# Optimization experiments

Hardware: AMD Instinct MI355X
Metric: run time of the kernel (lower is better)

The kernel has to match this reference:

```python
import jax, jax.numpy as jnp
import numpy as np

EPS = 1e-11
NUM_ITERATIONS = 3


def squash(t, axis=-1):
    # squared norm along axis, squash scale = |s|^2/(1+|s|^2)
    sq = jnp.sum(t * t, axis=axis, keepdims=True)
    scale = sq / (1.0 + sq)
    unit = t / jnp.sqrt(sq + EPS)
    return scale * unit, scale


def setup_inputs() -> dict:
    key = jax.random.key(0)
    kx, ka, kw, kal = jax.random.split(key, 4)
    B, Nl, Nh, Din, Dout, K = 32, 256, 16, 16, 32, 8
    x = jax.random.normal(kx, (B, Nl, Din, Din), dtype=jnp.float32)
    adj = jax.random.normal(ka, (B, Nl, Nl), dtype=jnp.float32)  # unused by forward
    W = jax.random.normal(kw, (K, Din, Dout), dtype=jnp.float32)
    alpha = jax.random.normal(kal, (Nl, Nh, K), dtype=jnp.float32)
    return {"x": x, "adj": adj, "W": W, "alpha": alpha}


def reference(x, adj, W, alpha):
    B, Nl, Din, _ = x.shape
    Nh = alpha.shape[1]
    Dout = W.shape[2]
    # tmp2 = sum_k W[k] * alpha[l,h,k]  -> (Nl, Nh, Din, Dout)
    tmp2 = jnp.einsum('kio,lhk->lhio', W, alpha)
    # u_hat: per lower-capsule matrix times transform -> (B, Nl, Nh, Din, Dout)
    u = jnp.einsum('blri,lhio->blhro', x, tmp2)
    D = Din * Dout
    u_hat = u.reshape(B, Nl, Nh, D)  # capsule vector dim flattened (trailing 1 dropped)

    # dynamic routing on detached u_hat
    uh = jax.lax.stop_gradient(u_hat)
    b = jnp.zeros((B, Nl, Nh, 1), dtype=u_hat.dtype)
    for _ in range(NUM_ITERATIONS - 1):
        c = jax.nn.softmax(b, axis=2)               # over higher capsules
        s = jnp.sum(c * uh, axis=1, keepdims=True)  # (B,1,Nh,D)
        v, _ = squash(s, axis=-1)
        b = b + jnp.sum(uh * v, axis=-1, keepdims=True)  # agreement u_hat^T v
    c = jax.nn.softmax(b, axis=2)

    # final weighted sum with non-detached u_hat
    s = jnp.sum(c * u_hat, axis=1, keepdims=True)   # (B,1,Nh,D)
    v, a = squash(s, axis=-1)
    # match original shapes: v (B,1,Nh,D,1), a_j (B,1,Nh,1,1)
    return v[..., None], a[..., None]
```

## Files before the change

### kernel.cpp

```cpp
#include <hip/hip_runtime.h>
#include <hip/hip_bf16.h>

#define B_     32
#define NL     256
#define NH     16
#define DD     512
#define KK     8
#define LPB    32
#define NLC    (NL / LPB)
#define CHUNK  4
#define PSTR   24

typedef _Float16 f16;
typedef __attribute__((ext_vector_type(8)))  f16   f16x8;
typedef __attribute__((ext_vector_type(16))) float f32x16;

#define LO_SCALE 1024.0f
#define LO_INV   (1.0f / 1024.0f)

__device__ __forceinline__ void split2s(float f, f16& h, f16& l) {
    h = (f16)f;
    l = (f16)((f - (float)h) * LO_SCALE);
}

__global__ __launch_bounds__(512)
void tmp2_kernel(const float* __restrict__ W, const float* __restrict__ alpha,
                 f16* __restrict__ t2h, f16* __restrict__ t2l) {
    const int lh = blockIdx.x, d = threadIdx.x;
    const float* a = alpha + lh * KK;
    float acc = 0.f;
#pragma unroll
    for (int k = 0; k < KK; ++k) acc = fmaf(a[k], W[k * DD + d], acc);
    f16 h, l; split2s(acc, h, l);
    const size_t tt = (size_t)lh * DD + (d & 31) * 16 + (d >> 5);
    t2h[tt] = h; t2l[tt] = l;
}

template <int MODE>
__global__ __launch_bounds__(64)
void reduce_kernel(const float* __restrict__ spart, float* __restrict__ vbuf,
                   float* __restrict__ out_v, float* __restrict__ out_a) {
    const int bh = blockIdx.x, t = threadIdx.x;
    const float cs = (MODE == 0) ? (1.0f / 16.0f) : 1.0f;
    float acc[8];
#pragma unroll
    for (int j = 0; j < 8; ++j) acc[j] = 0.f;
    for (int ls = 0; ls < NLC; ++ls) {
        const float* p = spart + ((size_t)ls * (B_ * NH) + bh) * DD + t * 8;
        const float4 u0 = *(const float4*)&p[0];
        const float4 u1 = *(const float4*)&p[4];
        acc[0] += u0.x; acc[1] += u0.y; acc[2] += u0.z; acc[3] += u0.w;
        acc[4] += u1.x; acc[5] += u1.y; acc[6] += u1.z; acc[7] += u1.w;
    }
#pragma unroll
    for (int j = 0; j < 8; ++j) acc[j] *= cs;
    float sq = 0.f;
#pragma unroll
    for (int j = 0; j < 8; ++j) sq = fmaf(acc[j], acc[j], sq);
#pragma unroll
    for (int mm = 1; mm < 64; mm <<= 1) sq += __shfl_xor(sq, mm, 64);
    const float scale = sq / (1.0f + sq);
    const float inv   = scale / sqrtf(sq + 1e-11f);
    float* po = (MODE == 2) ? (out_v + (size_t)bh * DD + t * 8)
                            : (vbuf + (size_t)bh * DD + t * 8);
#pragma unroll
    for (int j = 0; j < 8; ++j) po[j] = acc[j] * inv;
    if (MODE == 2 && t == 0) out_a[bh] = scale;
}

template <int MODE>
__global__ __launch_bounds__(1024)
void pass_kernel(const float* __restrict__ x,
                 const f16* __restrict__ t2h, const f16* __restrict__ t2l,
                 const float* __restrict__ vbuf, float* __restrict__ blog,
                 float* __restrict__ spart) {
    __shared__ __align__(16) f16 xsh[LPB * 16 * PSTR];
    __shared__ __align__(16) f16 xsl[LPB * 16 * PSTR];
    __shared__ float dotsL[2][CHUNK][16];

    const int t  = threadIdx.x;
    const int b  = blockIdx.x >> 3, lc = blockIdx.x & 7;
    const int l0 = lc * LPB;
    const int wv = t >> 6, lane = t & 63;
    const int o  = lane & 31, l5 = lane >> 5;
    const int i0 = l5 * 8;
    const int rA = lane & 15;

    {
        const int row = t >> 1, half = t & 1;
        const float* xg = x + ((size_t)b * NL + l0 + (row >> 4)) * 256
                            + (row & 15) * 16 + half * 8;
        float xv[8];
        *(float4*)&xv[0] = *(const float4*)&xg[0];
        *(float4*)&xv[4] = *(const float4*)&xg[4];
        f16 hi[8], lo[8];
#pragma unroll
        for (int j = 0; j < 8; ++j) split2s(xv[j], hi[j], lo[j]);
        const int la = row * PSTR + half * 8;
        *(f16x8*)&xsh[la] = *(f16x8*)&hi[0];
        *(f16x8*)&xsl[la] = *(f16x8*)&lo[0];
    }
    __syncthreads();

    float vr[8];
    if (MODE != 0) {
        const float* vp = vbuf + ((size_t)b * NH + wv) * DD;
#pragma unroll
        for (int j = 0; j < 8; ++j) {
            const int rr = (j & 3) + 8 * (j >> 2) + 4 * l5;
            vr[j] = vp[rr * 32 + o];
        }
    }

    f16x8 pf0, pf1;
    {
        const size_t tb = ((size_t)l0 * NH + wv) * DD + o * 16 + i0;
        pf0 = *(const f16x8*)(t2h + tb);
        pf1 = *(const f16x8*)(t2l + tb);
    }

    float sacc[8];
#pragma unroll
    for (int j = 0; j < 8; ++j) sacc[j] = 0.f;

    for (int ch = 0; ch < LPB / CHUNK; ++ch) {
        const int par = ch & 1;
        float blg = 0.f;
        if (MODE == 2)
            blg = blog[((size_t)b * NL + l0 + ch * CHUNK + (lane >> 4)) * NH + (lane & 15)];

        float Pst[CHUNK][8];
#pragma unroll
        for (int lq = 0; lq < CHUNK; ++lq) {
            const int l = ch * CHUNK + lq;
            const int la = (l * 16 + rA) * PSTR + i0;
            const f16x8 a0 = *(const f16x8*)&xsh[la];
            const f16x8 a1 = *(const f16x8*)&xsl[la];
            const f16x8 c0 = pf0, c1 = pf1;
            if (l + 1 < LPB) {
                const size_t tb = ((size_t)(l0 + l + 1) * NH + wv) * DD + o * 16 + i0;
                pf0 = *(const f16x8*)(t2h + tb);
                pf1 = *(const f16x8*)(t2l + tb);
            }
            f32x16 z;
#pragma unroll
            for (int j = 0; j < 16; ++j) z[j] = 0.f;
            f32x16 c00 = __builtin_amdgcn_mfma_f32_32x32x16_f16(a0, c0, z, 0, 0, 0);
            f32x16 c01 = __builtin_amdgcn_mfma_f32_32x32x16_f16(a0, c1, z, 0, 0, 0);
            f32x16 c10 = __builtin_amdgcn_mfma_f32_32x32x16_f16(a1, c0, z, 0, 0, 0);
            float d0 = 0.f;
#pragma unroll
            for (int j = 0; j < 8; ++j) {
                const float pj = fmaf(c01[j] + c10[j], LO_INV, c00[j]);
                if (MODE != 0) { Pst[lq][j] = pj; d0 = fmaf(pj, vr[j], d0); }
                else           sacc[j] += pj;
            }
            if (MODE != 0) {
#pragma unroll
                for (int mm = 1; mm < 64; mm <<= 1) d0 += __shfl_xor(d0, mm, 64);
                if (lane == 0) dotsL[par][lq][wv] = d0;
            }
        }

        if (MODE != 0) {
            __syncthreads();
            float d = dotsL[par][lane >> 4][lane & 15];
            if (MODE == 2) d += blg;
            if (MODE == 1 && wv == 0)
                blog[((size_t)b * NL + l0 + ch * CHUNK + (lane >> 4)) * NH + (lane & 15)] = d;
            float mx = d;
#pragma unroll
            for (int mm = 1; mm < 16; mm <<= 1) mx = fmaxf(mx, __shfl_xor(mx, mm, 16));
            const float e = __expf(d - mx);
            float sm = e;
#pragma unroll
            for (int mm = 1; mm < 16; mm <<= 1) sm += __shfl_xor(sm, mm, 16);
            const float cv = e / sm;
#pragma unroll
            for (int lq = 0; lq < CHUNK; ++lq) {
                const float c = __shfl(cv, lq * 16 + wv, 64);
#pragma unroll
                for (int j = 0; j < 8; ++j)
                    sacc[j] = fmaf(c, Pst[lq][j], sacc[j]);
            }
        }
    }

    {
        float* sp = spart + ((size_t)lc * (B_ * NH) + b * NH + wv) * DD;
#pragma unroll
        for (int j = 0; j < 8; ++j) {
            const int rr = (j & 3) + 8 * (j >> 2) + 4 * l5;
            sp[rr * 32 + o] = sacc[j];
        }
    }
}

extern "C" void kernel_launch(void* const* d_in, const int* in_sizes, int n_in,
                              void* d_out, int out_size, void* d_ws, size_t ws_size,
                              hipStream_t stream) {
    const float* x     = (const float*)d_in[0];
    const float* W     = (const float*)d_in[2];
    const float* alpha = (const float*)d_in[3];
    float* out   = (float*)d_out;
    float* out_v = out;
    float* out_a = out + (size_t)B_ * NH * DD;

    char* base = (char*)d_ws;
    size_t off = 0;
    f16*   t2h   = (f16*)(base + off);   off += (size_t)NL * NH * DD * 2;
    f16*   t2l   = (f16*)(base + off);   off += (size_t)NL * NH * DD * 2;
    float* spart = (float*)(base + off); off += (size_t)NLC * B_ * NH * DD * 4;
    float* vbuf  = (float*)(base + off); off += (size_t)B_ * NH * DD * 4;
    float* blogp = (float*)(base + off); off += (size_t)B_ * NL * NH * 4;

    tmp2_kernel<<<NL * NH, 512, 0, stream>>>(W, alpha, t2h, t2l);

    const int grid = B_ * NLC;
    pass_kernel<0><<<grid, 1024, 0, stream>>>(x, t2h, t2l, vbuf, blogp, spart);
    reduce_kernel<0><<<B_ * NH, 64, 0, stream>>>(spart, vbuf, nullptr, nullptr);

    pass_kernel<1><<<grid, 1024, 0, stream>>>(x, t2h, t2l, vbuf, blogp, spart);
    reduce_kernel<1><<<B_ * NH, 64, 0, stream>>>(spart, vbuf, nullptr, nullptr);

    pass_kernel<2><<<grid, 1024, 0, stream>>>(x, t2h, t2l, vbuf, blogp, spart);
    reduce_kernel<2><<<B_ * NH, 64, 0, stream>>>(spart, nullptr, out_v, out_a);
}
```

Before: 162.2 us.

## Fuse all routing passes into one persistent kernel with grid barriers

Replaces the seven separate launches (tmp2, three pass kernels, three reduce kernels) with a single persistent kernel of 256 blocks. Global atomic-counter barriers separate the tmp2 build, each routing pass and each squash reduction. Routing logits now stay in shared memory instead of a global buffer. The aim is to remove launch gaps and global round-trips, at the cost of relying on all 256 blocks being co-resident and paying for spin-wait barriers.

```diff
diff --git a/kernel.cpp b/kernel.cpp
--- a/kernel.cpp
+++ b/kernel.cpp
@@ -7,9 +7,10 @@
 #define DD     512
 #define KK     8
 #define LPB    32
-#define NLC    (NL / LPB)
+#define NLC    8
 #define CHUNK  4
 #define PSTR   24
+#define NBLK   256
 
 typedef _Float16 f16;
 typedef __attribute__((ext_vector_type(8)))  f16   f16x8;
@@ -23,68 +24,58 @@
     l = (f16)((f - (float)h) * LO_SCALE);
 }
 
-__global__ __launch_bounds__(512)
-void tmp2_kernel(const float* __restrict__ W, const float* __restrict__ alpha,
-                 f16* __restrict__ t2h, f16* __restrict__ t2l) {
-    const int lh = blockIdx.x, d = threadIdx.x;
-    const float* a = alpha + lh * KK;
-    float acc = 0.f;
-#pragma unroll
-    for (int k = 0; k < KK; ++k) acc = fmaf(a[k], W[k * DD + d], acc);
-    f16 h, l; split2s(acc, h, l);
-    const size_t tt = (size_t)lh * DD + (d & 31) * 16 + (d >> 5);
-    t2h[tt] = h; t2l[tt] = l;
-}
-
-template <int MODE>
-__global__ __launch_bounds__(64)
-void reduce_kernel(const float* __restrict__ spart, float* __restrict__ vbuf,
-                   float* __restrict__ out_v, float* __restrict__ out_a) {
-    const int bh = blockIdx.x, t = threadIdx.x;
-    const float cs = (MODE == 0) ? (1.0f / 16.0f) : 1.0f;
-    float acc[8];
-#pragma unroll
-    for (int j = 0; j < 8; ++j) acc[j] = 0.f;
-    for (int ls = 0; ls < NLC; ++ls) {
-        const float* p = spart + ((size_t)ls * (B_ * NH) + bh) * DD + t * 8;
-        const float4 u0 = *(const float4*)&p[0];
-        const float4 u1 = *(const float4*)&p[4];
-        acc[0] += u0.x; acc[1] += u0.y; acc[2] += u0.z; acc[3] += u0.w;
-        acc[4] += u1.x; acc[5] += u1.y; acc[6] += u1.z; acc[7] += u1.w;
-    }
-#pragma unroll
-    for (int j = 0; j < 8; ++j) acc[j] *= cs;
-    float sq = 0.f;
-#pragma unroll
-    for (int j = 0; j < 8; ++j) sq = fmaf(acc[j], acc[j], sq);
-#pragma unroll
-    for (int mm = 1; mm < 64; mm <<= 1) sq += __shfl_xor(sq, mm, 64);
-    const float scale = sq / (1.0f + sq);
-    const float inv   = scale / sqrtf(sq + 1e-11f);
-    float* po = (MODE == 2) ? (out_v + (size_t)bh * DD + t * 8)
-                            : (vbuf + (size_t)bh * DD + t * 8);
-#pragma unroll
-    for (int j = 0; j < 8; ++j) po[j] = acc[j] * inv;
-    if (MODE == 2 && t == 0) out_a[bh] = scale;
-}
-
-template <int MODE>
-__global__ __launch_bounds__(1024)
-void pass_kernel(const float* __restrict__ x,
-                 const f16* __restrict__ t2h, const f16* __restrict__ t2l,
-                 const float* __restrict__ vbuf, float* __restrict__ blog,
-                 float* __restrict__ spart) {
+__device__ __forceinline__ void gbar(unsigned* cnt, int id) {
+    __syncthreads();
+    if (threadIdx.x == 0) {
+        __threadfence();
+        atomicAdd(&cnt[id], 1u);
+        while (__hip_atomic_load(&cnt[id], __ATOMIC_RELAXED,
+                                 __HIP_MEMORY_SCOPE_AGENT) < NBLK)
+            __builtin_amdgcn_s_sleep(2);
+        __threadfence();
+    }
+    __syncthreads();
+}
+
+__global__ __launch_bounds__(1024, 4)
+void fused_kernel(const float* __restrict__ x, const float* __restrict__ W,
+                  const float* __restrict__ alpha,
+                  f16* __restrict__ t2h, f16* __restrict__ t2l,
+                  float* __restrict__ vbuf, float* __restrict__ spart,
+                  unsigned* __restrict__ cnt,
+                  float* __restrict__ out_v, float* __restrict__ out_a) {
     __shared__ __align__(16) f16 xsh[LPB * 16 * PSTR];
     __shared__ __align__(16) f16 xsl[LPB * 16 * PSTR];
     __shared__ float dotsL[2][CHUNK][16];
+    __shared__ float blogS[LPB][16];
 
     const int t  = threadIdx.x;
-    const int b  = blockIdx.x >> 3, lc = blockIdx.x & 7;
+    const int lc = blockIdx.x >> 5, b = blockIdx.x & 31;
     const int l0 = lc * LPB;
     const int wv = t >> 6, lane = t & 63;
     const int o  = lane & 31, l5 = lane >> 5;
     const int i0 = l5 * 8;
     const int rA = lane & 15;
+
+    {
+        const int l = lc * 32 + b;
+        const int d = t & 511;
+        float wr[KK];
+#pragma unroll
+        for (int k = 0; k < KK; ++k) wr[k] = W[k * DD + d];
+        const size_t tbase = (size_t)l * NH * DD + ((d & 31) * 16 + (d >> 5));
+#pragma unroll
+        for (int e = 0; e < 8; ++e) {
+            const int h = 2 * e + (t >> 9);
+            const float* al = alpha + ((size_t)l * NH + h) * KK;
+            float acc = 0.f;
+#pragma unroll
+            for (int k = 0; k < KK; ++k) acc = fmaf(al[k], wr[k], acc);
+            f16 hh, ll; split2s(acc, hh, ll);
+            t2h[tbase + (size_t)h * DD] = hh;
+            t2l[tbase + (size_t)h * DD] = ll;
+        }
+    }
 
     {
         const int row = t >> 1, half = t & 1;
@@ -100,99 +91,129 @@
         *(f16x8*)&xsh[la] = *(f16x8*)&hi[0];
         *(f16x8*)&xsl[la] = *(f16x8*)&lo[0];
     }
-    __syncthreads();
-
-    float vr[8];
-    if (MODE != 0) {
-        const float* vp = vbuf + ((size_t)b * NH + wv) * DD;
-#pragma unroll
-        for (int j = 0; j < 8; ++j) {
-            const int rr = (j & 3) + 8 * (j >> 2) + 4 * l5;
-            vr[j] = vp[rr * 32 + o];
-        }
-    }
-
-    f16x8 pf0, pf1;
-    {
-        const size_t tb = ((size_t)l0 * NH + wv) * DD + o * 16 + i0;
-        pf0 = *(const f16x8*)(t2h + tb);
-        pf1 = *(const f16x8*)(t2l + tb);
-    }
-
-    float sacc[8];
-#pragma unroll
-    for (int j = 0; j < 8; ++j) sacc[j] = 0.f;
-
-    for (int ch = 0; ch < LPB / CHUNK; ++ch) {
-        const int par = ch & 1;
-        float blg = 0.f;
-        if (MODE == 2)
-            blg = blog[((size_t)b * NL + l0 + ch * CHUNK + (lane >> 4)) * NH + (lane & 15)];
-
-        float Pst[CHUNK][8];
-#pragma unroll
-        for (int lq = 0; lq < CHUNK; ++lq) {
-            const int l = ch * CHUNK + lq;
-            const int la = (l * 16 + rA) * PSTR + i0;
-            const f16x8 a0 = *(const f16x8*)&xsh[la];
-            const f16x8 a1 = *(const f16x8*)&xsl[la];
-            const f16x8 c0 = pf0, c1 = pf1;
-            if (l + 1 < LPB) {
-                const size_t tb = ((size_t)(l0 + l + 1) * NH + wv) * DD + o * 16 + i0;
-                pf0 = *(const f16x8*)(t2h + tb);
-                pf1 = *(const f16x8*)(t2l + tb);
-            }
-            f32x16 z;
-#pragma unroll
-            for (int j = 0; j < 16; ++j) z[j] = 0.f;
-            f32x16 c00 = __builtin_amdgcn_mfma_f32_32x32x16_f16(a0, c0, z, 0, 0, 0);
-            f32x16 c01 = __builtin_amdgcn_mfma_f32_32x32x16_f16(a0, c1, z, 0, 0, 0);
-            f32x16 c10 = __builtin_amdgcn_mfma_f32_32x32x16_f16(a1, c0, z, 0, 0, 0);
-            float d0 = 0.f;
+    gbar(cnt, 0);
+
+    for (int it = 0; it < 3; ++it) {
+        float vr[8];
+        if (it > 0) {
+            const float* vp = vbuf + ((size_t)b * NH + wv) * DD;
 #pragma unroll
             for (int j = 0; j < 8; ++j) {
-                const float pj = fmaf(c01[j] + c10[j], LO_INV, c00[j]);
-                if (MODE != 0) { Pst[lq][j] = pj; d0 = fmaf(pj, vr[j], d0); }
-                else           sacc[j] += pj;
-            }
-            if (MODE != 0) {
-#pragma unroll
-                for (int mm = 1; mm < 64; mm <<= 1) d0 += __shfl_xor(d0, mm, 64);
-                if (lane == 0) dotsL[par][lq][wv] = d0;
-            }
-        }
-
-        if (MODE != 0) {
-            __syncthreads();
-            float d = dotsL[par][lane >> 4][lane & 15];
-            if (MODE == 2) d += blg;
-            if (MODE == 1 && wv == 0)
-                blog[((size_t)b * NL + l0 + ch * CHUNK + (lane >> 4)) * NH + (lane & 15)] = d;
-            float mx = d;
-#pragma unroll
-            for (int mm = 1; mm < 16; mm <<= 1) mx = fmaxf(mx, __shfl_xor(mx, mm, 16));
-            const float e = __expf(d - mx);
-            float sm = e;
-#pragma unroll
-            for (int mm = 1; mm < 16; mm <<= 1) sm += __shfl_xor(sm, mm, 16);
-            const float cv = e / sm;
+                const int rr = (j & 3) + 8 * (j >> 2) + 4 * l5;
+                vr[j] = vp[rr * 32 + o];
+            }
+        }
+
+        f16x8 pf0, pf1;
+        {
+            const size_t tb = ((size_t)l0 * NH + wv) * DD + o * 16 + i0;
+            pf0 = *(const f16x8*)(t2h + tb);
+            pf1 = *(const f16x8*)(t2l + tb);
+        }
+
+        float sacc[8];
+#pragma unroll
+        for (int j = 0; j < 8; ++j) sacc[j] = 0.f;
+
+        for (int ch = 0; ch < LPB / CHUNK; ++ch) {
+            const int par = ch & 1;
+            float Pst[CHUNK][8];
 #pragma unroll
             for (int lq = 0; lq < CHUNK; ++lq) {
-                const float c = __shfl(cv, lq * 16 + wv, 64);
-#pragma unroll
-                for (int j = 0; j < 8; ++j)
-                    sacc[j] = fmaf(c, Pst[lq][j], sacc[j]);
-            }
-        }
-    }
-
-    {
-        float* sp = spart + ((size_t)lc * (B_ * NH) + b * NH + wv) * DD;
-#pragma unroll
-        for (int j = 0; j < 8; ++j) {
-            const int rr = (j & 3) + 8 * (j >> 2) + 4 * l5;
-            sp[rr * 32 + o] = sacc[j];
-        }
+                const int l = ch * CHUNK + lq;
+                const int la = (l * 16 + rA) * PSTR + i0;
+                const f16x8 a0 = *(const f16x8*)&xsh[la];
+                const f16x8 a1 = *(const f16x8*)&xsl[la];
+                const f16x8 c0 = pf0, c1 = pf1;
+                if (l + 1 < LPB) {
+                    const size_t tb = ((size_t)(l0 + l + 1) * NH + wv) * DD + o * 16 + i0;
+                    pf0 = *(const f16x8*)(t2h + tb);
+                    pf1 = *(const f16x8*)(t2l + tb);
+                }
+                f32x16 z;
+#pragma unroll
+                for (int j = 0; j < 16; ++j) z[j] = 0.f;
+                f32x16 c00 = __builtin_amdgcn_mfma_f32_32x32x16_f16(a0, c0, z, 0, 0, 0);
+                f32x16 c01 = __builtin_amdgcn_mfma_f32_32x32x16_f16(a0, c1, z, 0, 0, 0);
+                f32x16 c10 = __builtin_amdgcn_mfma_f32_32x32x16_f16(a1, c0, z, 0, 0, 0);
+                float d0 = 0.f;
+#pragma unroll
+                for (int j = 0; j < 8; ++j) {
+                    const float pj = fmaf(c01[j] + c10[j], LO_INV, c00[j]);
+                    if (it != 0) { Pst[lq][j] = pj; d0 = fmaf(pj, vr[j], d0); }
+                    else         sacc[j] += pj;
+                }
+                if (it != 0) {
+#pragma unroll
+                    for (int mm = 1; mm < 64; mm <<= 1) d0 += __shfl_xor(d0, mm, 64);
+                    if (lane == 0) dotsL[par][lq][wv] = d0;
+                }
+            }
+
+            if (it != 0) {
+                __syncthreads();
+                const int lql = lane >> 4, hq = lane & 15;
+                float d = dotsL[par][lql][hq];
+                if (it == 2) d += blogS[ch * CHUNK + lql][hq];
+                if (it == 1 && wv == 0) blogS[ch * CHUNK + lql][hq] = d;
+                float mx = d;
+#pragma unroll
+                for (int mm = 1; mm < 16; mm <<= 1) mx = fmaxf(mx, __shfl_xor(mx, mm, 16));
+                const float e = __expf(d - mx);
+                float sm = e;
+#pragma unroll
+                for (int mm = 1; mm < 16; mm <<= 1) sm += __shfl_xor(sm, mm, 16);
+                const float cv = e / sm;
+#pragma unroll
+                for (int lq = 0; lq < CHUNK; ++lq) {
+                    const float c = __shfl(cv, lq * 16 + wv, 64);
+#pragma unroll
+                    for (int j = 0; j < 8; ++j)
+                        sacc[j] = fmaf(c, Pst[lq][j], sacc[j]);
+                }
+            }
+        }
+
+        {
+            float* sp = spart + ((size_t)lc * (B_ * NH) + b * NH + wv) * DD;
+#pragma unroll
+            for (int j = 0; j < 8; ++j) {
+                const int rr = (j & 3) + 8 * (j >> 2) + 4 * l5;
+                sp[rr * 32 + o] = sacc[j];
+            }
+        }
+        gbar(cnt, 1 + 2 * it);
+
+        if (wv < 2) {
+            const int h  = lc * 2 + wv;
+            const int bh = b * NH + h;
+            const float cs = (it == 0) ? (1.0f / 16.0f) : 1.0f;
+            float acc[8];
+#pragma unroll
+            for (int j = 0; j < 8; ++j) acc[j] = 0.f;
+            for (int ls = 0; ls < NLC; ++ls) {
+                const float* p = spart + ((size_t)ls * (B_ * NH) + bh) * DD + lane * 8;
+                const float4 u0 = *(const float4*)&p[0];
+                const float4 u1 = *(const float4*)&p[4];
+                acc[0] += u0.x; acc[1] += u0.y; acc[2] += u0.z; acc[3] += u0.w;
+                acc[4] += u1.x; acc[5] += u1.y; acc[6] += u1.z; acc[7] += u1.w;
+            }
+#pragma unroll
+            for (int j = 0; j < 8; ++j) acc[j] *= cs;
+            float sq = 0.f;
+#pragma unroll
+            for (int j = 0; j < 8; ++j) sq = fmaf(acc[j], acc[j], sq);
+#pragma unroll
+            for (int mm = 1; mm < 64; mm <<= 1) sq += __shfl_xor(sq, mm, 64);
+            const float scale = sq / (1.0f + sq);
+            const float inv   = scale / sqrtf(sq + 1e-11f);
+            float* po = (it == 2) ? (out_v + (size_t)bh * DD + lane * 8)
+                                  : (vbuf + (size_t)bh * DD + lane * 8);
+#pragma unroll
+            for (int j = 0; j < 8; ++j) po[j] = acc[j] * inv;
+            if (it == 2 && lane == 0) out_a[bh] = scale;
+        }
+        if (it < 2) gbar(cnt, 2 + 2 * it);
     }
 }
 
@@ -208,21 +229,14 @@
 
     char* base = (char*)d_ws;
     size_t off = 0;
-    f16*   t2h   = (f16*)(base + off);   off += (size_t)NL * NH * DD * 2;
-    f16*   t2l   = (f16*)(base + off);   off += (size_t)NL * NH * DD * 2;
-    float* spart = (float*)(base + off); off += (size_t)NLC * B_ * NH * DD * 4;
-    float* vbuf  = (float*)(base + off); off += (size_t)B_ * NH * DD * 4;
-    float* blogp = (float*)(base + off); off += (size_t)B_ * NL * NH * 4;
-
-    tmp2_kernel<<<NL * NH, 512, 0, stream>>>(W, alpha, t2h, t2l);
-
-    const int grid = B_ * NLC;
-    pass_kernel<0><<<grid, 1024, 0, stream>>>(x, t2h, t2l, vbuf, blogp, spart);
-    reduce_kernel<0><<<B_ * NH, 64, 0, stream>>>(spart, vbuf, nullptr, nullptr);
-
-    pass_kernel<1><<<grid, 1024, 0, stream>>>(x, t2h, t2l, vbuf, blogp, spart);
-    reduce_kernel<1><<<B_ * NH, 64, 0, stream>>>(spart, vbuf, nullptr, nullptr);
-
-    pass_kernel<2><<<grid, 1024, 0, stream>>>(x, t2h, t2l, vbuf, blogp, spart);
-    reduce_kernel<2><<<B_ * NH, 64, 0, stream>>>(spart, nullptr, out_v, out_a);
-}
+    f16*      t2h   = (f16*)(base + off);      off += (size_t)NL * NH * DD * 2;
+    f16*      t2l   = (f16*)(base + off);      off += (size_t)NL * NH * DD * 2;
+    float*    spart = (float*)(base + off);    off += (size_t)NLC * B_ * NH * DD * 4;
+    float*    vbuf  = (float*)(base + off);    off += (size_t)B_ * NH * DD * 4;
+    unsigned* cnt   = (unsigned*)(base + off); off += 64;
+
+    hipMemsetAsync(cnt, 0, 64, stream);
+
+    fused_kernel<<<NBLK, 1024, 0, stream>>>(x, W, alpha, t2h, t2l,
+                                            vbuf, spart, cnt, out_v, out_a);
+}
```

Measured after the change: 379.3 us. 2.34x slower.
